# Performance work log

Measured on AMD Instinct MI355X. Metric: run time of the kernel, lower is better.

## Reference

```python
import jax, jax.numpy as jnp
import numpy as np

# AE(N=32, C=27, in=64, inter=64, out=64, pool=(2,2), factor=1); eval mode
# (dropout = identity, BatchNorm uses running stats mean=0, var=1).
BT, CIN, F, COUT, NC, NG = 64, 64, 64, 64, 27, 32
L = NG * NG  # 1024 spatial nodes
EPS = 1e-5

def setup_inputs() -> dict:
    key = jax.random.key(0)
    ks = jax.random.split(key, 14)
    s = 0.05
    return {
        "x": jax.random.normal(ks[0], (BT, CIN, NG, NG), jnp.float32),
        "SP": jax.random.normal(ks[1], (BT, NC, 2 * NG, 2 * NG), jnp.float32),
        "trans_w": jax.random.normal(ks[2], (F, CIN), jnp.float32) * s,   # 1x1 conv, no bias
        "bn1_g": jnp.ones((F,), jnp.float32),
        "bn1_b": jnp.zeros((F,), jnp.float32),
        "w_nc": jax.random.normal(ks[3], (NC, L), jnp.float32) * s,       # Linear(N*N -> C)
        "b_nc": jnp.zeros((NC,), jnp.float32),
        "w_kc": jax.random.normal(ks[4], (NC, F), jnp.float32) * s,       # Linear(F -> C)
        "b_kc": jnp.zeros((NC,), jnp.float32),
        "w_g": jax.random.normal(ks[5], (F, F), jnp.float32) * s,         # GNN weight
        "b_g": jnp.zeros((F,), jnp.float32),
        "adj_sp": jax.random.normal(ks[6], (L, L), jnp.float32) * 0.01,   # SpatialGNN static adjacency
        "w_sp": jax.random.normal(ks[7], (F, F), jnp.float32) * s,        # SpatialGNN weight
        "b_sp": jnp.zeros((F,), jnp.float32),
        "back_w": jax.random.normal(ks[8], (COUT, F), jnp.float32) * s,   # 1x1 conv, no bias
        "bn2_g": jnp.ones((COUT,), jnp.float32),
        "bn2_b": jnp.zeros((COUT,), jnp.float32),
    }

def reference(x, SP, trans_w, bn1_g, bn1_b, w_nc, b_nc, w_kc, b_kc,
              w_g, b_g, adj_sp, w_sp, b_sp, back_w, bn2_g, bn2_b):
    # SP: softmax over classes, 2x2 maxpool, flatten -> [B, C, L]
    SPs = jax.nn.softmax(SP, axis=1)
    B, C, H, W = SPs.shape
    SPp = SPs.reshape(B, C, H // 2, 2, W // 2, 2).max(axis=(3, 5)).reshape(B, C, -1)
    # trans: 1x1 conv (no bias) + BN(eval: mean=0, var=1) + ReLU
    t = jnp.einsum('bchw,fc->bfhw', x, trans_w)
    sc1 = bn1_g / jnp.sqrt(1.0 + EPS)
    t = jax.nn.relu(t * sc1[None, :, None, None] + bn1_b[None, :, None, None])
    Bx, Ff, h, w = t.shape
    y = t.reshape(Bx, Ff, h * w)                                   # [B, F, L]
    # sigma = linearKC(linearNC(y).permute(0,2,1)) -> [B, C, C]
    yn = jnp.einsum('bfl,cl->bfc', y, w_nc) + b_nc                 # [B, F, C]
    sigma = jnp.einsum('bfc,kf->bck', yn, w_kc) + b_kc             # [B, C, C]
    # dynamic adjacency A = SP^T @ sigma @ SP -> [B, L, L]
    tmp = jnp.einsum('bck,bkm->bcm', sigma, SPp)                   # [B, C, L]
    A = jnp.einsum('bcl,bcm->blm', SPp, tmp)                       # [B, L, L]
    yt = y.transpose(0, 2, 1)                                      # [B, L, F]
    # GNN(A, y) + y : graph conv relu(A @ y @ W^T + b) with residual
    se = jax.nn.relu(jnp.einsum('blm,bmf->blf', A, yt) @ w_g.T + b_g) + yt
    # SpatialGNN(y) + y : static adjacency message passing
    sp = jax.nn.relu(jnp.einsum('lm,bmf->blf', adj_sp, yt) @ w_sp.T + b_sp) + yt
    y2 = se + sp                                                   # [B, L, F]
    # upsample(factor=1)=identity, dropout(eval)=identity, residual with t
    y2 = y2.transpose(0, 2, 1).reshape(Bx, Ff, h, w) + t
    # back: 1x1 conv (no bias) + BN(eval) + ReLU
    out = jnp.einsum('bfhw,of->bohw', y2, back_w)
    sc2 = bn2_g / jnp.sqrt(1.0 + EPS)
    out = jax.nn.relu(out * sc2[None, :, None, None] + bn2_b[None, :, None, None])
    return out
```

## Files before the change

### kernel.cpp

```cpp
#include <hip/hip_runtime.h>

#define B_  64
#define F_  64
#define NC_ 27
#define L_  1024
#define EPSV 1e-5f
#define NCHUNK 8

typedef __bf16 bf16x8 __attribute__((ext_vector_type(8)));
typedef float  f32x4  __attribute__((ext_vector_type(4)));

static __device__ __forceinline__ float relu_(float v) { return fmaxf(v, 0.f); }
static __device__ __forceinline__ ushort f2bf(float f) {
    __bf16 h = (__bf16)f;
    ushort r;
    __builtin_memcpy(&r, &h, 2);
    return r;
}
static __device__ __forceinline__ float bf2f(ushort u) {
    __bf16 h;
    __builtin_memcpy(&h, &u, 2);
    return (float)h;
}
static __device__ __forceinline__ bf16x8 cvt8(float4 a, float4 b) {
    bf16x8 r;
    r[0] = (__bf16)a.x; r[1] = (__bf16)a.y; r[2] = (__bf16)a.z; r[3] = (__bf16)a.w;
    r[4] = (__bf16)b.x; r[5] = (__bf16)b.y; r[6] = (__bf16)b.z; r[7] = (__bf16)b.w;
    return r;
}

__global__ __launch_bounds__(256) void k_mega(
    const float* __restrict__ x, const float* __restrict__ SP,
    const float* __restrict__ w, const float* __restrict__ g,
    const float* __restrict__ beta, const float* __restrict__ w_sp,
    const float* __restrict__ w_nc,
    const float* __restrict__ adj, const float* __restrict__ bw,
    const float* __restrict__ g2,
    ushort* __restrict__ Pt, ushort* __restrict__ yb16, ushort* __restrict__ ywb,
    float* __restrict__ partYN, float* __restrict__ partU,
    ushort* __restrict__ adjb, ushort* __restrict__ bwb)
{
    const int blk = blockIdx.x;
    const int t = threadIdx.x;
    if (blk >= 512) {
        if (blk < 1536) {
            int i = (((blk - 512) << 8) + t) << 2;
            float4 v = *(const float4*)(adj + i);
            ushort4 o;
            o.x = f2bf(v.x); o.y = f2bf(v.y); o.z = f2bf(v.z); o.w = f2bf(v.w);
            *(ushort4*)(adjb + i) = o;
        } else {
            const float rs = 1.f / sqrtf(1.f + EPSV);
            for (int j = t; j < 4096; j += 256) {
                int o = j >> 6;
                bwb[j] = f2bf(bw[j] * g2[o] * rs);
            }
        }
        return;
    }

    __shared__ __align__(16) char pool[47616];
    ushort* sT_  = (ushort*)pool;
    ushort* sTt_ = (ushort*)(pool + 18432);
    ushort* sP_  = (ushort*)(pool + 38912);
    float*  red  = (float*)pool;
#define ST(wv_, l_, f_)  sT_[((wv_) * 32 + (l_)) * 72 + (f_)]
#define STT(wv_, f_, l_) sTt_[((wv_) * 64 + (f_)) * 40 + (l_)]
#define SPD(c_, l_)      sP_[(c_) * 136 + (l_)]

    const int wv = t >> 6, lane = t & 63;
    const int rA = lane & 15, kg = lane >> 4;
    const int b = blk >> 3;
    const int l0 = (blk & 7) << 7;
    const int wl0 = l0 + wv * 32;

    {
        const int ll = t >> 1, sub = t & 1;
        const int ol = l0 + ll;
        const int oi = ol >> 5, oj = ol & 31;
        const float* rp = SP + (size_t)b * NC_ * 4096 + (2 * oi + sub) * 64 + 2 * oj;
        float v0[NC_], v1[NC_];
        float m0 = -1e30f, m1 = -1e30f;
#pragma unroll
        for (int c = 0; c < NC_; ++c) {
            float2 v = *(const float2*)(rp + c * 4096);
            v0[c] = v.x; v1[c] = v.y;
            m0 = fmaxf(m0, v.x); m1 = fmaxf(m1, v.y);
        }
        float s0 = 0.f, s1 = 0.f;
#pragma unroll
        for (int c = 0; c < NC_; ++c) {
            v0[c] = __expf(v0[c] - m0); s0 += v0[c];
            v1[c] = __expf(v1[c] - m1); s1 += v1[c];
        }
        float i0 = 1.f / s0, i1 = 1.f / s1;
        float acc[NC_];
#pragma unroll
        for (int c = 0; c < NC_; ++c) acc[c] = fmaxf(v0[c] * i0, v1[c] * i1);
#pragma unroll
        for (int c = 0; c < NC_; ++c) acc[c] = fmaxf(acc[c], __shfl_xor(acc[c], 1));
        if (!sub) {
            ushort h[32];
#pragma unroll
            for (int c = 0; c < NC_; ++c) { h[c] = f2bf(acc[c]); SPD(c, ll) = h[c]; }
#pragma unroll
            for (int c = NC_; c < 32; ++c) h[c] = 0;
            ushort* pt = Pt + ((size_t)b * L_ + ol) * 32;
#pragma unroll
            for (int c0 = 0; c0 < 32; c0 += 4)
                *(ushort4*)&pt[c0] = *(ushort4*)&h[c0];
        } else {
#pragma unroll
            for (int r = NC_; r < 32; ++r)
                for (int c = ll; c < 136; c += 128) SPD(r, c) = 0;
        }
    }

    const float* xb = x + ((size_t)b << 16);
    f32x4 acc[2][4];
#pragma unroll
    for (int i = 0; i < 2; ++i)
#pragma unroll
        for (int j = 0; j < 4; ++j) acc[i][j] = (f32x4){0.f, 0.f, 0.f, 0.f};
#pragma unroll
    for (int ks = 0; ks < 2; ++ks) {
        bf16x8 a[2];
#pragma unroll
        for (int lt = 0; lt < 2; ++lt) {
            const int l = wl0 + lt * 16 + rA;
            bf16x8 av;
#pragma unroll
            for (int j = 0; j < 8; ++j)
                av[j] = (__bf16)xb[(size_t)(ks * 32 + kg * 8 + j) * 1024 + l];
            a[lt] = av;
        }
#pragma unroll
        for (int fc = 0; fc < 4; ++fc) {
            const float* wp = w + (fc * 16 + rA) * 64 + ks * 32 + kg * 8;
            bf16x8 bv = cvt8(*(const float4*)wp, *(const float4*)(wp + 4));
            acc[0][fc] = __builtin_amdgcn_mfma_f32_16x16x32_bf16(a[0], bv, acc[0][fc], 0, 0, 0);
            acc[1][fc] = __builtin_amdgcn_mfma_f32_16x16x32_bf16(a[1], bv, acc[1][fc], 0, 0, 0);
        }
    }

    const float rs = 1.f / sqrtf(1.f + EPSV);
    ushort* yg = yb16 + ((size_t)b << 16);
#pragma unroll
    for (int fc = 0; fc < 4; ++fc) {
        const int f = fc * 16 + rA;
        const float sc = g[f] * rs, bb = beta[f];
#pragma unroll
        for (int lt = 0; lt < 2; ++lt) {
            ushort4 tv;
            ushort* tp = (ushort*)&tv;
#pragma unroll
            for (int r = 0; r < 4; ++r) {
                float v = relu_(sc * acc[lt][fc][r] + bb);
                tp[r] = f2bf(v);
                ST(wv, lt * 16 + kg * 4 + r, f) = tp[r];
                STT(wv, f, lt * 16 + kg * 4 + r) = tp[r];
            }
            *(ushort4*)(yg + (size_t)f * 1024 + wl0 + lt * 16 + kg * 4) = tv;
        }
    }
    __syncthreads();

    f32x4 acc2[2][4];
#pragma unroll
    for (int i = 0; i < 2; ++i)
#pragma unroll
        for (int j = 0; j < 4; ++j) acc2[i][j] = (f32x4){0.f, 0.f, 0.f, 0.f};
#pragma unroll
    for (int kh = 0; kh < 2; ++kh) {
        bf16x8 a[2];
#pragma unroll
        for (int lt = 0; lt < 2; ++lt)
            a[lt] = *(const bf16x8*)&ST(wv, lt * 16 + rA, kh * 32 + kg * 8);
#pragma unroll
        for (int fc = 0; fc < 4; ++fc) {
            const float* wp = w_sp + (fc * 16 + rA) * 64 + kh * 32 + kg * 8;
            bf16x8 bv = cvt8(*(const float4*)wp, *(const float4*)(wp + 4));
            acc2[0][fc] = __builtin_amdgcn_mfma_f32_16x16x32_bf16(a[0], bv, acc2[0][fc], 0, 0, 0);
            acc2[1][fc] = __builtin_amdgcn_mfma_f32_16x16x32_bf16(a[1], bv, acc2[1][fc], 0, 0, 0);
        }
    }
    ushort* yp = ywb + ((size_t)b << 16);
#pragma unroll
    for (int fc = 0; fc < 4; ++fc) {
        const int f = fc * 16 + rA;
#pragma unroll
        for (int lt = 0; lt < 2; ++lt) {
            ushort4 ov;
            ov.x = f2bf(acc2[lt][fc][0]);
            ov.y = f2bf(acc2[lt][fc][1]);
            ov.z = f2bf(acc2[lt][fc][2]);
            ov.w = f2bf(acc2[lt][fc][3]);
            *(ushort4*)(yp + (size_t)f * 1024 + wl0 + lt * 16 + kg * 4) = ov;
        }
    }

    f32x4 accU[2][4], accN[2][4];
    {
        const int lw = wv * 32 + kg * 8;
        bf16x8 aU[2], aN[2];
        aU[0] = *(const bf16x8*)&SPD(rA, lw);
        aU[1] = *(const bf16x8*)&SPD(16 + rA, lw);
        {
            const float* w0 = w_nc + (size_t)rA * 1024 + l0 + lw;
            aN[0] = cvt8(*(const float4*)w0, *(const float4*)(w0 + 4));
            if (16 + rA < NC_) {
                const float* w1 = w_nc + (size_t)(16 + rA) * 1024 + l0 + lw;
                aN[1] = cvt8(*(const float4*)w1, *(const float4*)(w1 + 4));
            } else {
                bf16x8 z;
#pragma unroll
                for (int j = 0; j < 8; ++j) z[j] = (__bf16)0.f;
                aN[1] = z;
            }
        }
#pragma unroll
        for (int i = 0; i < 2; ++i)
#pragma unroll
            for (int j = 0; j < 4; ++j) {
                accU[i][j] = (f32x4){0.f, 0.f, 0.f, 0.f};
                accN[i][j] = (f32x4){0.f, 0.f, 0.f, 0.f};
            }
#pragma unroll
        for (int nt = 0; nt < 4; ++nt) {
            bf16x8 bt = *(const bf16x8*)&STT(wv, nt * 16 + rA, kg * 8);
#pragma unroll
            for (int mt = 0; mt < 2; ++mt) {
                accU[mt][nt] = __builtin_amdgcn_mfma_f32_16x16x32_bf16(aU[mt], bt, accU[mt][nt], 0, 0, 0);
                accN[mt][nt] = __builtin_amdgcn_mfma_f32_16x16x32_bf16(aN[mt], bt, accN[mt][nt], 0, 0, 0);
            }
        }
    }

    const int chunk = blk & 7;
    float* pu = partU  + ((size_t)b * NCHUNK + chunk) * (NC_ * 64);
    float* py = partYN + ((size_t)b * NCHUNK + chunk) * (NC_ * 64);
    __syncthreads();
#pragma unroll
    for (int mt = 0; mt < 2; ++mt)
#pragma unroll
        for (int r = 0; r < 4; ++r) {
            const int c = mt * 16 + kg * 4 + r;
            if (c < NC_) {
#pragma unroll
                for (int nt = 0; nt < 4; ++nt)
                    red[wv * 1728 + c * 64 + nt * 16 + rA] = accU[mt][nt][r];
            }
        }
    __syncthreads();
    for (int idx = t; idx < NC_ * 64; idx += 256)
        pu[idx] = red[idx] + red[1728 + idx] + red[2 * 1728 + idx] + red[3 * 1728 + idx];
    __syncthreads();
#pragma unroll
    for (int mt = 0; mt < 2; ++mt)
#pragma unroll
        for (int r = 0; r < 4; ++r) {
            const int c = mt * 16 + kg * 4 + r;
            if (c < NC_) {
#pragma unroll
                for (int nt = 0; nt < 4; ++nt)
                    red[wv * 1728 + c * 64 + nt * 16 + rA] = accN[mt][nt][r];
            }
        }
    __syncthreads();
    for (int idx = t; idx < NC_ * 64; idx += 256)
        py[idx] = red[idx] + red[1728 + idx] + red[2 * 1728 + idx] + red[3 * 1728 + idx];
#undef ST
#undef STT
#undef SPD
}

__global__ void k_sigma_Z(const float* __restrict__ partYN, const float* __restrict__ partU,
                          const float* __restrict__ b_nc,
                          const float* __restrict__ w_kc, const float* __restrict__ b_kc,
                          const float* __restrict__ w_g, ushort* __restrict__ Zwt)
{
    __shared__ float syn[F_ * NC_];
    __shared__ float su[NC_ * F_];
    __shared__ float swkt[F_ * 28];
    __shared__ float ssig[NC_ * NC_];
    __shared__ float sz[NC_ * F_];
    __shared__ float swg[F_ * F_];
    const int t = threadIdx.x;
    const int b = blockIdx.x;
    for (int idx = t; idx < NC_ * F_; idx += 256) {
        int c = idx >> 6, f = idx & 63;
        float sy = 0.f, suv = 0.f;
        const float* py = partYN + ((size_t)b * NCHUNK) * (NC_ * 64) + idx;
        const float* pu = partU  + ((size_t)b * NCHUNK) * (NC_ * 64) + idx;
#pragma unroll
        for (int p = 0; p < NCHUNK; ++p) {
            sy  += py[p * (NC_ * 64)];
            suv += pu[p * (NC_ * 64)];
        }
        syn[f * NC_ + c] = sy + b_nc[c];
        su[c * F_ + f]   = suv;
    }
    for (int idx = t; idx < NC_ * F_; idx += 256) {
        int k = idx >> 6, ff = idx & 63;
        swkt[ff * 28 + k] = w_kc[idx];
    }
    for (int idx = t; idx < F_ * F_; idx += 256) swg[idx] = w_g[idx];
    __syncthreads();
    for (int idx = t; idx < NC_ * NC_; idx += 256) {
        int c = idx / NC_, k = idx - c * NC_;
        float s = b_kc[k];
        for (int ff = 0; ff < F_; ++ff)
            s = fmaf(syn[ff * NC_ + c], swkt[ff * 28 + k], s);
        ssig[c * NC_ + k] = s;
    }
    __syncthreads();
    for (int idx = t; idx < NC_ * F_; idx += 256) {
        int c = idx >> 6, ff = idx & 63;
        float s = 0.f;
        for (int k = 0; k < NC_; ++k)
            s = fmaf(ssig[c * NC_ + k], su[k * F_ + ff], s);
        sz[idx] = s;
    }
    __syncthreads();
    for (int idx = t; idx < F_ * 32; idx += 256) {
        int f = idx >> 5, c = idx & 31;
        float s = 0.f;
        if (c < NC_)
            for (int fp = 0; fp < F_; ++fp)
                s = fmaf(sz[c * F_ + fp], swg[f * F_ + fp], s);
        Zwt[(size_t)b * F_ * 32 + idx] = f2bf(s);
    }
}

__global__ __launch_bounds__(256, 2) void k_fused2(
    const ushort* __restrict__ adjb_, const ushort* __restrict__ ywb_,
    const ushort* __restrict__ Pt_, const ushort* __restrict__ Zwt_,
    const ushort* __restrict__ yb16, const float* __restrict__ b_g,
    const float* __restrict__ b_sp, const ushort* __restrict__ bwb_,
    const float* __restrict__ bn2b, float* __restrict__ out)
{
    __shared__ __align__(16) char pool[65536];
    ushort* sYW = (ushort*)pool;
    float*  sPre = (float*)pool;

    const int t = threadIdx.x;
    const int w = t >> 6, lane = t & 63;
    const int rA = lane & 15, kg = lane >> 4;
    const int fr = rA & 7;
    const int b = blockIdx.x >> 3;
    const int l0 = (blockIdx.x & 7) << 7;
    const int wl0 = l0 + w * 32;

    const __bf16* adjb = (const __bf16*)adjb_;
    const __bf16* ywb  = (const __bf16*)ywb_ + ((size_t)b << 16);
    const __bf16* Ptb  = (const __bf16*)Pt_  + ((size_t)b << 15);
    const __bf16* Zwtb = (const __bf16*)Zwt_ + ((size_t)b << 11);
    const __bf16* bwb  = (const __bf16*)bwb_;

    f32x4 accS[2][4];
#pragma unroll
    for (int i = 0; i < 2; ++i)
#pragma unroll
        for (int j = 0; j < 4; ++j) accS[i][j] = (f32x4){0.f, 0.f, 0.f, 0.f};

    const __bf16* pa = adjb + (size_t)(wl0 + rA) * 1024 + kg * 8;

    bf16x8 st[16];
#pragma unroll
    for (int i = 0; i < 16; ++i) {
        int q = i * 256 + t;
        int f = q >> 6, cm = q & 63;
        st[i] = *(const bf16x8*)(ywb + (size_t)f * 1024 + cm * 8);
    }
#pragma unroll
    for (int i = 0; i < 16; ++i) {
        int q = i * 256 + t;
        int f = q >> 6, cm = q & 63;
        *(bf16x8*)&sYW[f * 512 + ((cm ^ (f & 7)) << 3)] = st[i];
    }
    __syncthreads();
#pragma unroll
    for (int i = 0; i < 16; ++i) {
        int q = i * 256 + t;
        int f = q >> 6, cm = q & 63;
        st[i] = *(const bf16x8*)(ywb + (size_t)f * 1024 + 512 + cm * 8);
    }
#pragma unroll 4
    for (int ksl = 0; ksl < 16; ++ksl) {
        bf16x8 a0 = *(const bf16x8*)(pa + ksl * 32);
        bf16x8 a1 = *(const bf16x8*)(pa + 16 * 1024 + ksl * 32);
        const int ch = ((kg + ksl * 4) ^ fr) << 3;
        bf16x8 f0 = *(const bf16x8*)&sYW[(0 * 16 + rA) * 512 + ch];
        bf16x8 f1 = *(const bf16x8*)&sYW[(1 * 16 + rA) * 512 + ch];
        bf16x8 f2 = *(const bf16x8*)&sYW[(2 * 16 + rA) * 512 + ch];
        bf16x8 f3 = *(const bf16x8*)&sYW[(3 * 16 + rA) * 512 + ch];
        accS[0][0] = __builtin_amdgcn_mfma_f32_16x16x32_bf16(a0, f0, accS[0][0], 0, 0, 0);
        accS[0][1] = __builtin_amdgcn_mfma_f32_16x16x32_bf16(a0, f1, accS[0][1], 0, 0, 0);
        accS[0][2] = __builtin_amdgcn_mfma_f32_16x16x32_bf16(a0, f2, accS[0][2], 0, 0, 0);
        accS[0][3] = __builtin_amdgcn_mfma_f32_16x16x32_bf16(a0, f3, accS[0][3], 0, 0, 0);
        accS[1][0] = __builtin_amdgcn_mfma_f32_16x16x32_bf16(a1, f0, accS[1][0], 0, 0, 0);
        accS[1][1] = __builtin_amdgcn_mfma_f32_16x16x32_bf16(a1, f1, accS[1][1], 0, 0, 0);
        accS[1][2] = __builtin_amdgcn_mfma_f32_16x16x32_bf16(a1, f2, accS[1][2], 0, 0, 0);
        accS[1][3] = __builtin_amdgcn_mfma_f32_16x16x32_bf16(a1, f3, accS[1][3], 0, 0, 0);
    }
    __syncthreads();
#pragma unroll
    for (int i = 0; i < 16; ++i) {
        int q = i * 256 + t;
        int f = q >> 6, cm = q & 63;
        *(bf16x8*)&sYW[f * 512 + ((cm ^ (f & 7)) << 3)] = st[i];
    }
    __syncthreads();
#pragma unroll 4
    for (int ksl = 0; ksl < 16; ++ksl) {
        bf16x8 a0 = *(const bf16x8*)(pa + (16 + ksl) * 32);
        bf16x8 a1 = *(const bf16x8*)(pa + 16 * 1024 + (16 + ksl) * 32);
        const int ch = ((kg + ksl * 4) ^ fr) << 3;
        bf16x8 f0 = *(const bf16x8*)&sYW[(0 * 16 + rA) * 512 + ch];
        bf16x8 f1 = *(const bf16x8*)&sYW[(1 * 16 + rA) * 512 + ch];
        bf16x8 f2 = *(const bf16x8*)&sYW[(2 * 16 + rA) * 512 + ch];
        bf16x8 f3 = *(const bf16x8*)&sYW[(3 * 16 + rA) * 512 + ch];
        accS[0][0] = __builtin_amdgcn_mfma_f32_16x16x32_bf16(a0, f0, accS[0][0], 0, 0, 0);
        accS[0][1] = __builtin_amdgcn_mfma_f32_16x16x32_bf16(a0, f1, accS[0][1], 0, 0, 0);
        accS[0][2] = __builtin_amdgcn_mfma_f32_16x16x32_bf16(a0, f2, accS[0][2], 0, 0, 0);
        accS[0][3] = __builtin_amdgcn_mfma_f32_16x16x32_bf16(a0, f3, accS[0][3], 0, 0, 0);
        accS[1][0] = __builtin_amdgcn_mfma_f32_16x16x32_bf16(a1, f0, accS[1][0], 0, 0, 0);
        accS[1][1] = __builtin_amdgcn_mfma_f32_16x16x32_bf16(a1, f1, accS[1][1], 0, 0, 0);
        accS[1][2] = __builtin_amdgcn_mfma_f32_16x16x32_bf16(a1, f2, accS[1][2], 0, 0, 0);
        accS[1][3] = __builtin_amdgcn_mfma_f32_16x16x32_bf16(a1, f3, accS[1][3], 0, 0, 0);
    }
    __syncthreads();

    f32x4 accD[2][4];
#pragma unroll
    for (int i = 0; i < 2; ++i)
#pragma unroll
        for (int j = 0; j < 4; ++j) accD[i][j] = (f32x4){0.f, 0.f, 0.f, 0.f};
    {
        const __bf16* qa = Ptb + (size_t)(wl0 + rA) * 32 + kg * 8;
        bf16x8 a0 = *(const bf16x8*)(qa);
        bf16x8 a1 = *(const bf16x8*)(qa + 16 * 32);
        const __bf16* qb = Zwtb + (size_t)rA * 32 + kg * 8;
        bf16x8 z0 = *(const bf16x8*)(qb + 0 * 512);
        bf16x8 z1 = *(const bf16x8*)(qb + 1 * 512);
        bf16x8 z2 = *(const bf16x8*)(qb + 2 * 512);
        bf16x8 z3 = *(const bf16x8*)(qb + 3 * 512);
        accD[0][0] = __builtin_amdgcn_mfma_f32_16x16x32_bf16(a0, z0, accD[0][0], 0, 0, 0);
        accD[0][1] = __builtin_amdgcn_mfma_f32_16x16x32_bf16(a0, z1, accD[0][1], 0, 0, 0);
        accD[0][2] = __builtin_amdgcn_mfma_f32_16x16x32_bf16(a0, z2, accD[0][2], 0, 0, 0);
        accD[0][3] = __builtin_amdgcn_mfma_f32_16x16x32_bf16(a0, z3, accD[0][3], 0, 0, 0);
        accD[1][0] = __builtin_amdgcn_mfma_f32_16x16x32_bf16(a1, z0, accD[1][0], 0, 0, 0);
        accD[1][1] = __builtin_amdgcn_mfma_f32_16x16x32_bf16(a1, z1, accD[1][1], 0, 0, 0);
        accD[1][2] = __builtin_amdgcn_mfma_f32_16x16x32_bf16(a1, z2, accD[1][2], 0, 0, 0);
        accD[1][3] = __builtin_amdgcn_mfma_f32_16x16x32_bf16(a1, z3, accD[1][3], 0, 0, 0);
    }

    float bg4[4], bs4[4];
#pragma unroll
    for (int fc = 0; fc < 4; ++fc) { bg4[fc] = b_g[fc * 16 + rA]; bs4[fc] = b_sp[fc * 16 + rA]; }
    const ushort* yb = yb16 + ((size_t)b << 16);
    const int wOff = w * 32 * 68;
#pragma unroll
    for (int lt = 0; lt < 2; ++lt) {
        int lbase = wl0 + lt * 16 + kg * 4;
        int row = lt * 16 + kg * 4;
#pragma unroll
        for (int fc = 0; fc < 4; ++fc) {
            int f = fc * 16 + rA;
            ushort4 uy = *(const ushort4*)(yb + (size_t)f * 1024 + lbase);
            const float ya[4] = {bf2f(uy.x), bf2f(uy.y), bf2f(uy.z), bf2f(uy.w)};
            f32x4 s = accS[lt][fc], d = accD[lt][fc];
            sPre[wOff + (row + 0) * 68 + f] = relu_(d[0] + bg4[fc]) + relu_(s[0] + bs4[fc]) + 3.f * ya[0];
            sPre[wOff + (row + 1) * 68 + f] = relu_(d[1] + bg4[fc]) + relu_(s[1] + bs4[fc]) + 3.f * ya[1];
            sPre[wOff + (row + 2) * 68 + f] = relu_(d[2] + bg4[fc]) + relu_(s[2] + bs4[fc]) + 3.f * ya[2];
            sPre[wOff + (row + 3) * 68 + f] = relu_(d[3] + bg4[fc]) + relu_(s[3] + bs4[fc]) + 3.f * ya[3];
        }
    }
    __syncthreads();

    f32x4 accO[2][4];
#pragma unroll
    for (int i = 0; i < 2; ++i)
#pragma unroll
        for (int j = 0; j < 4; ++j) accO[i][j] = (f32x4){0.f, 0.f, 0.f, 0.f};
#pragma unroll
    for (int kh = 0; kh < 2; ++kh) {
        bf16x8 af[2];
#pragma unroll
        for (int lt = 0; lt < 2; ++lt) {
            int off = wOff + (lt * 16 + rA) * 68 + kh * 32 + kg * 8;
            float4 u0 = *(const float4*)&sPre[off];
            float4 u1 = *(const float4*)&sPre[off + 4];
            bf16x8 a;
            a[0] = (__bf16)u0.x; a[1] = (__bf16)u0.y; a[2] = (__bf16)u0.z; a[3] = (__bf16)u0.w;
            a[4] = (__bf16)u1.x; a[5] = (__bf16)u1.y; a[6] = (__bf16)u1.z; a[7] = (__bf16)u1.w;
            af[lt] = a;
        }
#pragma unroll
        for (int oc = 0; oc < 4; ++oc) {
            bf16x8 bo = *(const bf16x8*)(bwb + oc * 1024 + (size_t)rA * 64 + kh * 32 + kg * 8);
            accO[0][oc] = __builtin_amdgcn_mfma_f32_16x16x32_bf16(af[0], bo, accO[0][oc], 0, 0, 0);
            accO[1][oc] = __builtin_amdgcn_mfma_f32_16x16x32_bf16(af[1], bo, accO[1][oc], 0, 0, 0);
        }
    }
    float* ob = out + ((size_t)b << 16);
#pragma unroll
    for (int oc = 0; oc < 4; ++oc) {
        float b2v = bn2b[oc * 16 + rA];
#pragma unroll
        for (int lt = 0; lt < 2; ++lt) {
            float4 ov = make_float4(accO[lt][oc][0] + b2v, accO[lt][oc][1] + b2v,
                                    accO[lt][oc][2] + b2v, accO[lt][oc][3] + b2v);
            ov.x = relu_(ov.x); ov.y = relu_(ov.y); ov.z = relu_(ov.z); ov.w = relu_(ov.w);
            *(float4*)(ob + (size_t)(oc * 16 + rA) * 1024 + wl0 + lt * 16 + kg * 4) = ov;
        }
    }
}

extern "C" void kernel_launch(void* const* d_in, const int* in_sizes, int n_in,
                              void* d_out, int out_size, void* d_ws, size_t ws_size,
                              hipStream_t stream)
{
    const float* x       = (const float*)d_in[0];
    const float* SP      = (const float*)d_in[1];
    const float* trans_w = (const float*)d_in[2];
    const float* bn1_g   = (const float*)d_in[3];
    const float* bn1_b   = (const float*)d_in[4];
    const float* w_nc    = (const float*)d_in[5];
    const float* b_nc    = (const float*)d_in[6];
    const float* w_kc    = (const float*)d_in[7];
    const float* b_kc    = (const float*)d_in[8];
    const float* w_g     = (const float*)d_in[9];
    const float* b_g     = (const float*)d_in[10];
    const float* adj     = (const float*)d_in[11];
    const float* w_sp    = (const float*)d_in[12];
    const float* b_sp    = (const float*)d_in[13];
    const float* back_w  = (const float*)d_in[14];
    const float* bn2_g   = (const float*)d_in[15];
    const float* bn2_b   = (const float*)d_in[16];
    float* out = (float*)d_out;

    float* ws = (float*)d_ws;
    float* partYN = ws;
    float* partU  = partYN + (size_t)B_ * NCHUNK * NC_ * F_;
    ushort* Pt   = (ushort*)(partU + (size_t)B_ * NCHUNK * NC_ * F_);
    ushort* Zwt  = Pt   + (size_t)B_ * L_ * 32;
    ushort* yb16 = Zwt  + (size_t)B_ * F_ * 32;
    ushort* ywb  = yb16 + (size_t)B_ * F_ * L_;
    ushort* adjb = ywb  + (size_t)B_ * F_ * L_;
    ushort* bwb  = adjb + (size_t)L_ * L_;

    k_mega<<<1537, 256, 0, stream>>>(x, SP, trans_w, bn1_g, bn1_b, w_sp, w_nc,
                                     adj, back_w, bn2_g,
                                     Pt, yb16, ywb, partYN, partU, adjb, bwb);
    k_sigma_Z<<<64, 256, 0, stream>>>(partYN, partU, b_nc, w_kc, b_kc, w_g, Zwt);
    k_fused2<<<512, 256, 0, stream>>>(adjb, ywb, Pt, Zwt, yb16, b_g, b_sp, bwb, bn2_b, out);
}
```

Before: 84.43 us.

## Halve k_fused2 row tile, stage Y in four LDS chunks, double grid

k_fused2 now handles 64 spatial rows per block instead of 128, with each wave owning 16 rows. The Y tile is staged in four 256-column LDS chunks with register prefetch, so LDS drops to 32KB and launch bounds allow 4 blocks per CU over a 1024-block grid. The goal is more occupancy and parallelism, at the cost of each block re-reading the full per-batch Y slab twice as often overall. k_sigma_Z is also launched with 512 threads instead of 256.

```diff
diff --git a/kernel.cpp b/kernel.cpp
--- a/kernel.cpp
+++ b/kernel.cpp
@@ -287,7 +287,7 @@
     __shared__ float swg[F_ * F_];
     const int t = threadIdx.x;
     const int b = blockIdx.x;
-    for (int idx = t; idx < NC_ * F_; idx += 256) {
+    for (int idx = t; idx < NC_ * F_; idx += 512) {
         int c = idx >> 6, f = idx & 63;
         float sy = 0.f, suv = 0.f;
         const float* py = partYN + ((size_t)b * NCHUNK) * (NC_ * 64) + idx;
@@ -300,13 +300,13 @@
         syn[f * NC_ + c] = sy + b_nc[c];
         su[c * F_ + f]   = suv;
     }
-    for (int idx = t; idx < NC_ * F_; idx += 256) {
+    for (int idx = t; idx < NC_ * F_; idx += 512) {
         int k = idx >> 6, ff = idx & 63;
         swkt[ff * 28 + k] = w_kc[idx];
     }
-    for (int idx = t; idx < F_ * F_; idx += 256) swg[idx] = w_g[idx];
-    __syncthreads();
-    for (int idx = t; idx < NC_ * NC_; idx += 256) {
+    for (int idx = t; idx < F_ * F_; idx += 512) swg[idx] = w_g[idx];
+    __syncthreads();
+    for (int idx = t; idx < NC_ * NC_; idx += 512) {
         int c = idx / NC_, k = idx - c * NC_;
         float s = b_kc[k];
         for (int ff = 0; ff < F_; ++ff)
@@ -314,7 +314,7 @@
         ssig[c * NC_ + k] = s;
     }
     __syncthreads();
-    for (int idx = t; idx < NC_ * F_; idx += 256) {
+    for (int idx = t; idx < NC_ * F_; idx += 512) {
         int c = idx >> 6, ff = idx & 63;
         float s = 0.f;
         for (int k = 0; k < NC_; ++k)
@@ -322,7 +322,7 @@
         sz[idx] = s;
     }
     __syncthreads();
-    for (int idx = t; idx < F_ * 32; idx += 256) {
+    for (int idx = t; idx < F_ * 32; idx += 512) {
         int f = idx >> 5, c = idx & 31;
         float s = 0.f;
         if (c < NC_)
@@ -332,14 +332,14 @@
     }
 }
 
-__global__ __launch_bounds__(256, 2) void k_fused2(
+__global__ __launch_bounds__(256, 4) void k_fused2(
     const ushort* __restrict__ adjb_, const ushort* __restrict__ ywb_,
     const ushort* __restrict__ Pt_, const ushort* __restrict__ Zwt_,
     const ushort* __restrict__ yb16, const float* __restrict__ b_g,
     const float* __restrict__ b_sp, const ushort* __restrict__ bwb_,
     const float* __restrict__ bn2b, float* __restrict__ out)
 {
-    __shared__ __align__(16) char pool[65536];
+    __shared__ __align__(16) char pool[32768];
     ushort* sYW = (ushort*)pool;
     float*  sPre = (float*)pool;
 
@@ -347,9 +347,9 @@
     const int w = t >> 6, lane = t & 63;
     const int rA = lane & 15, kg = lane >> 4;
     const int fr = rA & 7;
-    const int b = blockIdx.x >> 3;
-    const int l0 = (blockIdx.x & 7) << 7;
-    const int wl0 = l0 + w * 32;
+    const int b = blockIdx.x >> 4;
+    const int l0 = (blockIdx.x & 15) << 6;
+    const int wl0 = l0 + w * 16;
 
     const __bf16* adjb = (const __bf16*)adjb_;
     const __bf16* ywb  = (const __bf16*)ywb_ + ((size_t)b << 16);
@@ -357,163 +357,123 @@
     const __bf16* Zwtb = (const __bf16*)Zwt_ + ((size_t)b << 11);
     const __bf16* bwb  = (const __bf16*)bwb_;
 
-    f32x4 accS[2][4];
-#pragma unroll
-    for (int i = 0; i < 2; ++i)
-#pragma unroll
-        for (int j = 0; j < 4; ++j) accS[i][j] = (f32x4){0.f, 0.f, 0.f, 0.f};
+    f32x4 accS[4];
+#pragma unroll
+    for (int j = 0; j < 4; ++j) accS[j] = (f32x4){0.f, 0.f, 0.f, 0.f};
 
     const __bf16* pa = adjb + (size_t)(wl0 + rA) * 1024 + kg * 8;
 
-    bf16x8 st[16];
-#pragma unroll
-    for (int i = 0; i < 16; ++i) {
-        int q = i * 256 + t;
-        int f = q >> 6, cm = q & 63;
+    bf16x8 st[8];
+#pragma unroll
+    for (int i = 0; i < 8; ++i) {
+        int idx = i * 256 + t;
+        int f = idx >> 5, cm = idx & 31;
         st[i] = *(const bf16x8*)(ywb + (size_t)f * 1024 + cm * 8);
     }
 #pragma unroll
-    for (int i = 0; i < 16; ++i) {
-        int q = i * 256 + t;
-        int f = q >> 6, cm = q & 63;
-        *(bf16x8*)&sYW[f * 512 + ((cm ^ (f & 7)) << 3)] = st[i];
-    }
-    __syncthreads();
-#pragma unroll
-    for (int i = 0; i < 16; ++i) {
-        int q = i * 256 + t;
-        int f = q >> 6, cm = q & 63;
-        st[i] = *(const bf16x8*)(ywb + (size_t)f * 1024 + 512 + cm * 8);
-    }
-#pragma unroll 4
-    for (int ksl = 0; ksl < 16; ++ksl) {
-        bf16x8 a0 = *(const bf16x8*)(pa + ksl * 32);
-        bf16x8 a1 = *(const bf16x8*)(pa + 16 * 1024 + ksl * 32);
-        const int ch = ((kg + ksl * 4) ^ fr) << 3;
-        bf16x8 f0 = *(const bf16x8*)&sYW[(0 * 16 + rA) * 512 + ch];
-        bf16x8 f1 = *(const bf16x8*)&sYW[(1 * 16 + rA) * 512 + ch];
-        bf16x8 f2 = *(const bf16x8*)&sYW[(2 * 16 + rA) * 512 + ch];
-        bf16x8 f3 = *(const bf16x8*)&sYW[(3 * 16 + rA) * 512 + ch];
-        accS[0][0] = __builtin_amdgcn_mfma_f32_16x16x32_bf16(a0, f0, accS[0][0], 0, 0, 0);
-        accS[0][1] = __builtin_amdgcn_mfma_f32_16x16x32_bf16(a0, f1, accS[0][1], 0, 0, 0);
-        accS[0][2] = __builtin_amdgcn_mfma_f32_16x16x32_bf16(a0, f2, accS[0][2], 0, 0, 0);
-        accS[0][3] = __builtin_amdgcn_mfma_f32_16x16x32_bf16(a0, f3, accS[0][3], 0, 0, 0);
-        accS[1][0] = __builtin_amdgcn_mfma_f32_16x16x32_bf16(a1, f0, accS[1][0], 0, 0, 0);
-        accS[1][1] = __builtin_amdgcn_mfma_f32_16x16x32_bf16(a1, f1, accS[1][1], 0, 0, 0);
-        accS[1][2] = __builtin_amdgcn_mfma_f32_16x16x32_bf16(a1, f2, accS[1][2], 0, 0, 0);
-        accS[1][3] = __builtin_amdgcn_mfma_f32_16x16x32_bf16(a1, f3, accS[1][3], 0, 0, 0);
-    }
-    __syncthreads();
-#pragma unroll
-    for (int i = 0; i < 16; ++i) {
-        int q = i * 256 + t;
-        int f = q >> 6, cm = q & 63;
-        *(bf16x8*)&sYW[f * 512 + ((cm ^ (f & 7)) << 3)] = st[i];
-    }
-    __syncthreads();
-#pragma unroll 4
-    for (int ksl = 0; ksl < 16; ++ksl) {
-        bf16x8 a0 = *(const bf16x8*)(pa + (16 + ksl) * 32);
-        bf16x8 a1 = *(const bf16x8*)(pa + 16 * 1024 + (16 + ksl) * 32);
-        const int ch = ((kg + ksl * 4) ^ fr) << 3;
-        bf16x8 f0 = *(const bf16x8*)&sYW[(0 * 16 + rA) * 512 + ch];
-        bf16x8 f1 = *(const bf16x8*)&sYW[(1 * 16 + rA) * 512 + ch];
-        bf16x8 f2 = *(const bf16x8*)&sYW[(2 * 16 + rA) * 512 + ch];
-        bf16x8 f3 = *(const bf16x8*)&sYW[(3 * 16 + rA) * 512 + ch];
-        accS[0][0] = __builtin_amdgcn_mfma_f32_16x16x32_bf16(a0, f0, accS[0][0], 0, 0, 0);
-        accS[0][1] = __builtin_amdgcn_mfma_f32_16x16x32_bf16(a0, f1, accS[0][1], 0, 0, 0);
-        accS[0][2] = __builtin_amdgcn_mfma_f32_16x16x32_bf16(a0, f2, accS[0][2], 0, 0, 0);
-        accS[0][3] = __builtin_amdgcn_mfma_f32_16x16x32_bf16(a0, f3, accS[0][3], 0, 0, 0);
-        accS[1][0] = __builtin_amdgcn_mfma_f32_16x16x32_bf16(a1, f0, accS[1][0], 0, 0, 0);
-        accS[1][1] = __builtin_amdgcn_mfma_f32_16x16x32_bf16(a1, f1, accS[1][1], 0, 0, 0);
-        accS[1][2] = __builtin_amdgcn_mfma_f32_16x16x32_bf16(a1, f2, accS[1][2], 0, 0, 0);
-        accS[1][3] = __builtin_amdgcn_mfma_f32_16x16x32_bf16(a1, f3, accS[1][3], 0, 0, 0);
-    }
-    __syncthreads();
-
-    f32x4 accD[2][4];
-#pragma unroll
-    for (int i = 0; i < 2; ++i)
-#pragma unroll
-        for (int j = 0; j < 4; ++j) accD[i][j] = (f32x4){0.f, 0.f, 0.f, 0.f};
+    for (int i = 0; i < 8; ++i) {
+        int idx = i * 256 + t;
+        int f = idx >> 5, cm = idx & 31;
+        *(bf16x8*)&sYW[f * 256 + ((cm ^ (f & 7)) << 3)] = st[i];
+    }
+    __syncthreads();
+
+#pragma unroll
+    for (int q = 0; q < 4; ++q) {
+        if (q < 3) {
+#pragma unroll
+            for (int i = 0; i < 8; ++i) {
+                int idx = i * 256 + t;
+                int f = idx >> 5, cm = idx & 31;
+                st[i] = *(const bf16x8*)(ywb + (size_t)f * 1024 + (q + 1) * 256 + cm * 8);
+            }
+        }
+#pragma unroll
+        for (int ksl = 0; ksl < 8; ++ksl) {
+            const int ks = q * 8 + ksl;
+            bf16x8 a0 = *(const bf16x8*)(pa + ks * 32);
+            const int ch = ((ksl * 4 + kg) ^ fr) << 3;
+            bf16x8 f0 = *(const bf16x8*)&sYW[(0 * 16 + rA) * 256 + ch];
+            bf16x8 f1 = *(const bf16x8*)&sYW[(1 * 16 + rA) * 256 + ch];
+            bf16x8 f2 = *(const bf16x8*)&sYW[(2 * 16 + rA) * 256 + ch];
+            bf16x8 f3 = *(const bf16x8*)&sYW[(3 * 16 + rA) * 256 + ch];
+            accS[0] = __builtin_amdgcn_mfma_f32_16x16x32_bf16(a0, f0, accS[0], 0, 0, 0);
+            accS[1] = __builtin_amdgcn_mfma_f32_16x16x32_bf16(a0, f1, accS[1], 0, 0, 0);
+            accS[2] = __builtin_amdgcn_mfma_f32_16x16x32_bf16(a0, f2, accS[2], 0, 0, 0);
+            accS[3] = __builtin_amdgcn_mfma_f32_16x16x32_bf16(a0, f3, accS[3], 0, 0, 0);
+        }
+        __syncthreads();
+        if (q < 3) {
+#pragma unroll
+            for (int i = 0; i < 8; ++i) {
+                int idx = i * 256 + t;
+                int f = idx >> 5, cm = idx & 31;
+                *(bf16x8*)&sYW[f * 256 + ((cm ^ (f & 7)) << 3)] = st[i];
+            }
+            __syncthreads();
+        }
+    }
+
+    f32x4 accD[4];
+#pragma unroll
+    for (int j = 0; j < 4; ++j) accD[j] = (f32x4){0.f, 0.f, 0.f, 0.f};
     {
         const __bf16* qa = Ptb + (size_t)(wl0 + rA) * 32 + kg * 8;
         bf16x8 a0 = *(const bf16x8*)(qa);
-        bf16x8 a1 = *(const bf16x8*)(qa + 16 * 32);
         const __bf16* qb = Zwtb + (size_t)rA * 32 + kg * 8;
         bf16x8 z0 = *(const bf16x8*)(qb + 0 * 512);
         bf16x8 z1 = *(const bf16x8*)(qb + 1 * 512);
         bf16x8 z2 = *(const bf16x8*)(qb + 2 * 512);
         bf16x8 z3 = *(const bf16x8*)(qb + 3 * 512);
-        accD[0][0] = __builtin_amdgcn_mfma_f32_16x16x32_bf16(a0, z0, accD[0][0], 0, 0, 0);
-        accD[0][1] = __builtin_amdgcn_mfma_f32_16x16x32_bf16(a0, z1, accD[0][1], 0, 0, 0);
-        accD[0][2] = __builtin_amdgcn_mfma_f32_16x16x32_bf16(a0, z2, accD[0][2], 0, 0, 0);
-        accD[0][3] = __builtin_amdgcn_mfma_f32_16x16x32_bf16(a0, z3, accD[0][3], 0, 0, 0);
-        accD[1][0] = __builtin_amdgcn_mfma_f32_16x16x32_bf16(a1, z0, accD[1][0], 0, 0, 0);
-        accD[1][1] = __builtin_amdgcn_mfma_f32_16x16x32_bf16(a1, z1, accD[1][1], 0, 0, 0);
-        accD[1][2] = __builtin_amdgcn_mfma_f32_16x16x32_bf16(a1, z2, accD[1][2], 0, 0, 0);
-        accD[1][3] = __builtin_amdgcn_mfma_f32_16x16x32_bf16(a1, z3, accD[1][3], 0, 0, 0);
-    }
-
-    float bg4[4], bs4[4];
-#pragma unroll
-    for (int fc = 0; fc < 4; ++fc) { bg4[fc] = b_g[fc * 16 + rA]; bs4[fc] = b_sp[fc * 16 + rA]; }
+        accD[0] = __builtin_amdgcn_mfma_f32_16x16x32_bf16(a0, z0, accD[0], 0, 0, 0);
+        accD[1] = __builtin_amdgcn_mfma_f32_16x16x32_bf16(a0, z1, accD[1], 0, 0, 0);
+        accD[2] = __builtin_amdgcn_mfma_f32_16x16x32_bf16(a0, z2, accD[2], 0, 0, 0);
+        accD[3] = __builtin_amdgcn_mfma_f32_16x16x32_bf16(a0, z3, accD[3], 0, 0, 0);
+    }
+
     const ushort* yb = yb16 + ((size_t)b << 16);
-    const int wOff = w * 32 * 68;
-#pragma unroll
-    for (int lt = 0; lt < 2; ++lt) {
-        int lbase = wl0 + lt * 16 + kg * 4;
-        int row = lt * 16 + kg * 4;
-#pragma unroll
-        for (int fc = 0; fc < 4; ++fc) {
-            int f = fc * 16 + rA;
-            ushort4 uy = *(const ushort4*)(yb + (size_t)f * 1024 + lbase);
-            const float ya[4] = {bf2f(uy.x), bf2f(uy.y), bf2f(uy.z), bf2f(uy.w)};
-            f32x4 s = accS[lt][fc], d = accD[lt][fc];
-            sPre[wOff + (row + 0) * 68 + f] = relu_(d[0] + bg4[fc]) + relu_(s[0] + bs4[fc]) + 3.f * ya[0];
-            sPre[wOff + (row + 1) * 68 + f] = relu_(d[1] + bg4[fc]) + relu_(s[1] + bs4[fc]) + 3.f * ya[1];
-            sPre[wOff + (row + 2) * 68 + f] = relu_(d[2] + bg4[fc]) + relu_(s[2] + bs4[fc]) + 3.f * ya[2];
-            sPre[wOff + (row + 3) * 68 + f] = relu_(d[3] + bg4[fc]) + relu_(s[3] + bs4[fc]) + 3.f * ya[3];
-        }
-    }
-    __syncthreads();
-
-    f32x4 accO[2][4];
-#pragma unroll
-    for (int i = 0; i < 2; ++i)
-#pragma unroll
-        for (int j = 0; j < 4; ++j) accO[i][j] = (f32x4){0.f, 0.f, 0.f, 0.f};
+    const int wOff = w * 16 * 68;
+#pragma unroll
+    for (int fc = 0; fc < 4; ++fc) {
+        const int f = fc * 16 + rA;
+        const float bg = b_g[f], bs = b_sp[f];
+        const int lbase = wl0 + kg * 4;
+        const int row = kg * 4;
+        ushort4 uy = *(const ushort4*)(yb + (size_t)f * 1024 + lbase);
+        const float ya[4] = {bf2f(uy.x), bf2f(uy.y), bf2f(uy.z), bf2f(uy.w)};
+        f32x4 s = accS[fc], d = accD[fc];
+        sPre[wOff + (row + 0) * 68 + f] = relu_(d[0] + bg) + relu_(s[0] + bs) + 3.f * ya[0];
+        sPre[wOff + (row + 1) * 68 + f] = relu_(d[1] + bg) + relu_(s[1] + bs) + 3.f * ya[1];
+        sPre[wOff + (row + 2) * 68 + f] = relu_(d[2] + bg) + relu_(s[2] + bs) + 3.f * ya[2];
+        sPre[wOff + (row + 3) * 68 + f] = relu_(d[3] + bg) + relu_(s[3] + bs) + 3.f * ya[3];
+    }
+    __syncthreads();
+
+    f32x4 accO[4];
+#pragma unroll
+    for (int j = 0; j < 4; ++j) accO[j] = (f32x4){0.f, 0.f, 0.f, 0.f};
 #pragma unroll
     for (int kh = 0; kh < 2; ++kh) {
-        bf16x8 af[2];
-#pragma unroll
-        for (int lt = 0; lt < 2; ++lt) {
-            int off = wOff + (lt * 16 + rA) * 68 + kh * 32 + kg * 8;
-            float4 u0 = *(const float4*)&sPre[off];
-            float4 u1 = *(const float4*)&sPre[off + 4];
-            bf16x8 a;
-            a[0] = (__bf16)u0.x; a[1] = (__bf16)u0.y; a[2] = (__bf16)u0.z; a[3] = (__bf16)u0.w;
-            a[4] = (__bf16)u1.x; a[5] = (__bf16)u1.y; a[6] = (__bf16)u1.z; a[7] = (__bf16)u1.w;
-            af[lt] = a;
-        }
+        const int off = wOff + rA * 68 + kh * 32 + kg * 8;
+        float4 u0 = *(const float4*)&sPre[off];
+        float4 u1 = *(const float4*)&sPre[off + 4];
+        bf16x8 af;
+        af[0] = (__bf16)u0.x; af[1] = (__bf16)u0.y; af[2] = (__bf16)u0.z; af[3] = (__bf16)u0.w;
+        af[4] = (__bf16)u1.x; af[5] = (__bf16)u1.y; af[6] = (__bf16)u1.z; af[7] = (__bf16)u1.w;
 #pragma unroll
         for (int oc = 0; oc < 4; ++oc) {
             bf16x8 bo = *(const bf16x8*)(bwb + oc * 1024 + (size_t)rA * 64 + kh * 32 + kg * 8);
-            accO[0][oc] = __builtin_amdgcn_mfma_f32_16x16x32_bf16(af[0], bo, accO[0][oc], 0, 0, 0);
-            accO[1][oc] = __builtin_amdgcn_mfma_f32_16x16x32_bf16(af[1], bo, accO[1][oc], 0, 0, 0);
+            accO[oc] = __builtin_amdgcn_mfma_f32_16x16x32_bf16(af, bo, accO[oc], 0, 0, 0);
         }
     }
     float* ob = out + ((size_t)b << 16);
 #pragma unroll
     for (int oc = 0; oc < 4; ++oc) {
         float b2v = bn2b[oc * 16 + rA];
-#pragma unroll
-        for (int lt = 0; lt < 2; ++lt) {
-            float4 ov = make_float4(accO[lt][oc][0] + b2v, accO[lt][oc][1] + b2v,
-                                    accO[lt][oc][2] + b2v, accO[lt][oc][3] + b2v);
-            ov.x = relu_(ov.x); ov.y = relu_(ov.y); ov.z = relu_(ov.z); ov.w = relu_(ov.w);
-            *(float4*)(ob + (size_t)(oc * 16 + rA) * 1024 + wl0 + lt * 16 + kg * 4) = ov;
-        }
+        float4 ov = make_float4(accO[oc][0] + b2v, accO[oc][1] + b2v,
+                                accO[oc][2] + b2v, accO[oc][3] + b2v);
+        ov.x = relu_(ov.x); ov.y = relu_(ov.y); ov.z = relu_(ov.z); ov.w = relu_(ov.w);
+        *(float4*)(ob + (size_t)(oc * 16 + rA) * 1024 + wl0 + kg * 4) = ov;
     }
 }
 
@@ -553,6 +513,6 @@
     k_mega<<<1537, 256, 0, stream>>>(x, SP, trans_w, bn1_g, bn1_b, w_sp, w_nc,
                                      adj, back_w, bn2_g,
                                      Pt, yb16, ywb, partYN, partU, adjb, bwb);
-    k_sigma_Z<<<64, 256, 0, stream>>>(partYN, partU, b_nc, w_kc, b_kc, w_g, Zwt);
-    k_fused2<<<512, 256, 0, stream>>>(adjb, ywb, Pt, Zwt, yb16, b_g, b_sp, bwb, bn2_b, out);
-}
+    k_sigma_Z<<<64, 512, 0, stream>>>(partYN, partU, b_nc, w_kc, b_kc, w_g, Zwt);
+    k_fused2<<<1024, 256, 0, stream>>>(adjb, ywb, Pt, Zwt, yb16, b_g, b_sp, bwb, bn2_b, out);
+}
```

After: 77.32 us. -8.4%, faster.
